# Optimization experiments

Measured on AMD Instinct MI355X. Metric: run time of the kernel, lower is better.

Reference implementation:

```python
import jax, jax.numpy as jnp
import numpy as np

GROUPS = [16, 16, 32, 64, 192]
B, H, W = 8, 64, 64


def _shift(x, dy, dx):
    # out[i, j] = x[i - dy, j - dx], zero padded (equiv. of PoolConv's depthwise shift convs)
    Hh, Ww = x.shape[-2], x.shape[-1]
    pt, pb = max(dy, 0), max(-dy, 0)
    pl, pr = max(dx, 0), max(-dx, 0)
    xp = jnp.pad(x, ((0, 0), (0, 0), (pt, pb), (pl, pr)))
    return xp[..., pb:pb + Hh, pr:pr + Ww]


def _conv5(x, w, b):
    out = jax.lax.conv_general_dilated(x, w, (1, 1), ((2, 2), (2, 2)),
                                       dimension_numbers=("NCHW", "OIHW", "NCHW"))
    return out + b[None, :, None, None]


def _fill_pool(x, m1):
    # bottom: w[0,0]=1, pad 1 -> shift down-right; top: w[2,0]=1 -> shift up-right; right: w[2,0] of 5x5, pad 2 -> shift right by 2
    xm = x * m1
    return x + _shift(xm, 1, 1) + _shift(xm, -1, 1) + _shift(xm, 0, 2)


def _forward(y, mask, sws, sbs, cws, cbs):
    m0, m1 = mask[0], mask[1]
    starts = np.cumsum([0] + GROUPS[:-1])
    outs = []
    prev = None
    for i, g in enumerate(GROUPS):
        s = y[:, int(starts[i]):int(starts[i]) + g]
        anchor = _fill_pool(s * m0, m1)
        sp = _conv5(anchor, sws[i], sbs[i]) * (1.0 - m0)
        if i == 0:
            outs.append(sp)
            prev = s
        else:
            ch = _conv5(prev, cws[i - 1], cbs[i - 1])
            outs.append(sp)
            outs.append(ch)
            prev = jnp.concatenate([prev, s], axis=1)
    return tuple(outs)


def setup_inputs() -> dict:
    key = jax.random.key(0)
    ks = jax.random.split(key, 32)
    y = jax.random.normal(ks[0], (B, sum(GROUPS), H, W), jnp.float32)
    hh, ww = jnp.meshgrid(jnp.arange(H), jnp.arange(W), indexing="ij")
    m0 = (((hh + ww) % 2) == 0).astype(jnp.float32)[None, None]  # checkerboard anchor mask
    mask = jnp.stack([m0, 1.0 - m0], axis=0)  # [2,1,1,H,W]
    starts = np.cumsum([0] + GROUPS[:-1])
    inp = {"y": y, "mask": mask, "stage": 1}
    for i, g in enumerate(GROUPS):
        inp[f"sw{i}"] = 0.02 * jax.random.normal(ks[1 + i], (2 * g, g, 5, 5), jnp.float32)
        inp[f"sb{i}"] = jnp.zeros((2 * g,), jnp.float32)
    for i in range(1, len(GROUPS)):
        inp[f"cw{i}"] = 0.02 * jax.random.normal(ks[10 + i], (2 * GROUPS[i], int(starts[i]), 5, 5), jnp.float32)
        inp[f"cb{i}"] = jnp.zeros((2 * GROUPS[i],), jnp.float32)
    return inp


def reference(y, mask, stage, sw0, sb0, sw1, sb1, sw2, sb2, sw3, sb3, sw4, sb4,
              cw1, cb1, cw2, cb2, cw3, cb3, cw4, cb4):
    # stage != TRAIN branch: AdaptiveContext returns only the conv output
    return _forward(y, mask,
                    [sw0, sw1, sw2, sw3, sw4], [sb0, sb1, sb2, sb3, sb4],
                    [cw1, cw2, cw3, cw4], [cb1, cb2, cb3, cb4])
```

## Files before the change

kernel.cpp:

```cpp
#include <hip/hip_runtime.h>

typedef __bf16 bf16_t;
typedef __bf16 bf16x8 __attribute__((ext_vector_type(8)));
typedef float f32x16 __attribute__((ext_vector_type(16)));
typedef unsigned int u32;

#define CTOT 320
#define NPIX 32768

__device__ __forceinline__ void gload16(const void* g, void* l) {
  __builtin_amdgcn_global_load_lds((const __attribute__((address_space(1))) u32*)g,
                                   (__attribute__((address_space(3))) u32*)l, 16, 0, 0);
}

__global__ __launch_bounds__(256) void k_transpose_y(const float* __restrict__ y,
                                                     bf16_t* __restrict__ yt,
                                                     bf16_t* __restrict__ ytp) {
  __shared__ bf16_t T[64][72];
  int blk = blockIdx.x;
  int c0 = (blk % 5) * 64;
  int bh = blk / 5;
  int b = bh >> 6, h = bh & 63;
  int tid = threadIdx.x;
  {
    int c = tid >> 2, w0 = (tid & 3) << 4;
    const float* src = y + (size_t)(b * CTOT + c0 + c) * 4096 + (h << 6) + w0;
#pragma unroll
    for (int j = 0; j < 16; j += 4) {
      float4 v = *(const float4*)(src + j);
      T[c][w0 + j + 0] = (bf16_t)v.x;
      T[c][w0 + j + 1] = (bf16_t)v.y;
      T[c][w0 + j + 2] = (bf16_t)v.z;
      T[c][w0 + j + 3] = (bf16_t)v.w;
    }
  }
  __syncthreads();
  {
    int w = tid >> 2, cq = (tid & 3) << 4;
    union { uint4 v; bf16_t b[8]; } u0, u1;
#pragma unroll
    for (int j = 0; j < 8; ++j) { u0.b[j] = T[cq + j][w]; u1.b[j] = T[cq + 8 + j][w]; }
    bf16_t* dst = yt + (size_t)((bh << 6) | w) * CTOT + c0 + cq;
    *(uint4*)dst = u0.v;
    *(uint4*)(dst + 8) = u1.v;
  }
  if (tid < 128) {
    int j = tid >> 2, cq = (tid & 3) << 4;
    int w = (j << 1) + (h & 1);
    union { uint4 v; bf16_t b[8]; } u0, u1;
#pragma unroll
    for (int k = 0; k < 8; ++k) { u0.b[k] = T[cq + k][w]; u1.b[k] = T[cq + 8 + k][w]; }
    bf16_t* dst = ytp + (size_t)((bh << 5) + j) * CTOT + c0 + cq;
    *(uint4*)dst = u0.v;
    *(uint4*)(dst + 8) = u1.v;
  }
}

__global__ __launch_bounds__(256) void k_transpose_w(const float* __restrict__ w,
                                                     bf16_t* __restrict__ wt,
                                                     int IC, int OC, int OCp) {
  int idx = blockIdx.x * 256 + threadIdx.x;
  if (idx >= OCp * IC) return;
  int oc = idx / IC, ic = idx - oc * IC;
  bool valid = (oc < OC);
  const float* src = w + (size_t)(oc * IC + ic) * 25;
  int icg = ic >> 3, ie = ic & 7;
#pragma unroll
  for (int t = 0; t < 25; ++t) {
    float v = valid ? src[t] : 0.0f;
    wt[(size_t)((t * (IC >> 3) + icg) * OCp + oc) * 8 + ie] = (bf16_t)v;
  }
}

__global__ void k_zero(uint4* z) { z[threadIdx.x] = uint4{0u, 0u, 0u, 0u}; }

struct ConvDesc {
  const float* bias;
  int out_off, wt_off;
  int IC, OC, OCp, chs, masked, job_start;
};
struct MainParams {
  const bf16_t* yt;
  const bf16_t* ytp;
  const bf16_t* wt;
  const bf16_t* zp;
  float* out;
  ConvDesc cv[9];
};

template <bool MASKED>
__device__ __forceinline__ void conv_run(const ConvDesc cd, const MainParams& P,
                                         int local, bf16_t* S) {
  constexpr int COLS = MASKED ? 36 : 68;
  constexpr int REAL = MASKED ? 720 : 816;
  constexpr int NSG  = MASKED ? 12 : 13;
  constexpr int SPL  = NSG * 512;
  constexpr int SINB = 2 * SPL;
  constexpr int SWO  = 2 * SINB;

  int mb = MASKED ? (local >> 5) : (local >> 6);
  int nb = local & (MASKED ? 31 : 63);
  int b  = MASKED ? (nb >> 2) : (nb >> 3);
  int hblk = MASKED ? ((nb & 3) << 4) : ((nb & 7) << 3);
  int tid = threadIdx.x, lane = tid & 63, wid = tid >> 6;
  int l31 = lane & 31, kq = lane >> 5;

  int octmax = (cd.OC - (mb << 6)) >> 5; if (octmax > 2) octmax = 2;

  f32x16 acc00 = {}, acc01 = {}, acc10 = {}, acc11 = {};

  int aofs = SWO + kq * 512 + l31 * 8;
  int bofs = kq * SPL + (MASKED ? (((wid << 1) * 36 + 1 + l31) * 8)
                                : ((wid * 68 + l31) * 8));

  const bf16_t* wtc = P.wt + cd.wt_off;
  int icgs = cd.IC >> 3;
  int nchunks = cd.IC >> 4;

  auto stage_sin = [&](int cb, int buf) {
    int ic0 = cb << 4;
    for (int g = wid; g < 2 * NSG; g += 8) {
      int p = (g >= NSG) ? 1 : 0;
      int gi = g - p * NSG;
      int s = (gi << 6) + lane;
      int rr = s / COLS, cc = s - rr * COLS;
      int h = hblk + rr - 2;
      const bf16_t* gp;
      if (!MASKED) {
        int w = cc - 2;
        bool inb = (s < REAL) && ((unsigned)h < 64u) && ((unsigned)w < 64u);
        gp = inb ? (P.yt + (size_t)((((b << 6) + (h & 63)) << 6) | (w & 63)) * CTOT
                        + cd.chs + ic0 + (p << 3))
                 : P.zp;
      } else {
        int j = cc - 1;
        bool inb = (s < REAL) && ((unsigned)h < 64u) && ((unsigned)j < 32u);
        gp = inb ? (P.ytp + (size_t)((((b << 6) + (h & 63)) << 5) + (j & 31)) * CTOT
                         + cd.chs + ic0 + (p << 3))
                 : P.zp;
      }
      gload16(gp, S + buf * SINB + p * SPL + (gi << 9));
    }
  };
  auto stage_sw = [&](int gstart, int gcnt, int swb, int cb) {
    int ic0 = cb << 4;
    for (int t = wid; t < 2 * gcnt; t += 8) {
      int slot = t >> 1, icg = t & 1;
      int ti = gstart + slot;
      int tap = MASKED ? (2 * ti + 1) : ti;
      const bf16_t* gp = wtc +
          (size_t)((tap * icgs + (ic0 >> 3) + icg) * cd.OCp + (mb << 6) + lane) * 8;
      gload16(gp, S + SWO + ((swb * 7 + slot) << 10) + (icg << 9));
    }
  };

#define TAP_ONE(TI, SL)                                                         \
    {                                                                           \
      int tap_ = MASKED ? (2 * (TI) + 1) : (TI);                                \
      int dy_ = tap_ / 5, dx_ = tap_ % 5;                                       \
      bf16x8 af0 = *(const bf16x8*)(S + aofs + (SL) * 1024);                    \
      bf16x8 bf0, bf1;                                                          \
      if (!MASKED) {                                                            \
        int toff_ = (dy_ * 68 + dx_) * 8;                                       \
        bf0 = *(const bf16x8*)(Sn + bofs + toff_);                              \
        bf1 = *(const bf16x8*)(Sn + bofs + toff_ + 256);                        \
      } else {                                                                  \
        int j0_ = (dx_ - 1 - (dy_ & 1)) / 2;                                    \
        int j1_ = (dx_ - 2 - ((dy_ + 1) & 1)) / 2;                              \
        bf0 = *(const bf16x8*)(Sn + bofs + (dy_ * 36 + j0_) * 8);               \
        bf1 = *(const bf16x8*)(Sn + bofs + ((dy_ + 1) * 36 + j1_) * 8);         \
      }                                                                         \
      acc00 = __builtin_amdgcn_mfma_f32_32x32x16_bf16(af0, bf0, acc00, 0, 0, 0);\
      acc01 = __builtin_amdgcn_mfma_f32_32x32x16_bf16(af0, bf1, acc01, 0, 0, 0);\
      if (octmax > 1) {                                                         \
        bf16x8 af1 = *(const bf16x8*)(S + aofs + (SL) * 1024 + 256);            \
        acc10 = __builtin_amdgcn_mfma_f32_32x32x16_bf16(af1, bf0, acc10, 0,0,0);\
        acc11 = __builtin_amdgcn_mfma_f32_32x32x16_bf16(af1, bf1, acc11, 0,0,0);\
      }                                                                         \
    }
#define RUNG(GS, SB, CNT)                                                       \
    _Pragma("unroll")                                                           \
    for (int s_ = 0; s_ < (CNT); ++s_) TAP_ONE((GS) + s_, (SB) + s_)

  stage_sin(0, 0);
  stage_sw(0, MASKED ? 6 : 7, 0, 0);
  for (int cb = 0; cb < nchunks; ++cb) {
    const bf16_t* Sn = S + (cb & 1) * SINB;
    __syncthreads();
    if (!MASKED) {
      stage_sw(7, 6, 1, cb);
      RUNG(0, 0, 7)
      __syncthreads();
      stage_sw(13, 6, 0, cb);
      RUNG(7, 7, 6)
      __syncthreads();
      stage_sw(19, 6, 1, cb);
      RUNG(13, 0, 6)
      __syncthreads();
      if (cb + 1 < nchunks) {
        stage_sin(cb + 1, (cb + 1) & 1);
        stage_sw(0, 7, 0, cb + 1);
      }
      RUNG(19, 7, 6)
    } else {
      stage_sw(6, 6, 1, cb);
      RUNG(0, 0, 6)
      __syncthreads();
      if (cb + 1 < nchunks) {
        stage_sin(cb + 1, (cb + 1) & 1);
        stage_sw(0, 6, 0, cb + 1);
      }
      RUNG(6, 7, 6)
    }
  }
#undef RUNG
#undef TAP_ONE

  float* outp = P.out + cd.out_off;
#define EPI_U(A, OT, PT)                                                        \
  {                                                                             \
    int h = hblk + wid;                                                         \
    _Pragma("unroll")                                                           \
    for (int r = 0; r < 16; ++r) {                                              \
      int row = (r & 3) + ((r >> 2) << 3) + (kq << 2);                          \
      int oc = (mb << 6) + ((OT) << 5) + row;                                   \
      outp[(size_t)(b * cd.OC + oc) * 4096 + (h << 6) + ((PT) << 5) + l31] =    \
          (A)[r] + cd.bias[oc];                                                 \
    }                                                                           \
  }
#define EPI_M(A, OT, PT)                                                        \
  {                                                                             \
    int h = hblk + (wid << 1) + (PT);                                           \
    _Pragma("unroll")                                                           \
    for (int r = 0; r < 16; ++r) {                                              \
      int row = (r & 3) + ((r >> 2) << 3) + (kq << 2);                          \
      int oc = (mb << 6) + ((OT) << 5) + row;                                   \
      float val = (A)[r] + cd.bias[oc];                                         \
      float2 pr;                                                                \
      if ((PT) == 0) { pr.x = 0.0f; pr.y = val; }                               \
      else           { pr.x = val;  pr.y = 0.0f; }                              \
      *(float2*)(outp + (size_t)(b * cd.OC + oc) * 4096 + (h << 6) + (l31 << 1)) = pr; \
    }                                                                           \
  }
  if (!MASKED) {
    EPI_U(acc00, 0, 0); EPI_U(acc01, 0, 1);
    if (octmax > 1) { EPI_U(acc10, 1, 0); EPI_U(acc11, 1, 1); }
  } else {
    EPI_M(acc00, 0, 0); EPI_M(acc01, 0, 1);
    if (octmax > 1) { EPI_M(acc10, 1, 0); EPI_M(acc11, 1, 1); }
  }
#undef EPI_U
#undef EPI_M
}

__global__ __launch_bounds__(512, 4) void k_conv_main(MainParams P) {
  __shared__ bf16_t S[40960];
  int bid = blockIdx.x;
  int ci = 0;
#pragma unroll
  for (int i = 1; i < 9; ++i) if (bid >= P.cv[i].job_start) ci = i;
  ConvDesc cd = P.cv[ci];
  int local = bid - cd.job_start;
  if (cd.masked) conv_run<true>(cd, P, local, S);
  else           conv_run<false>(cd, P, local, S);
}

extern "C" void kernel_launch(void* const* d_in, const int* in_sizes, int n_in,
                              void* d_out, int out_size, void* d_ws, size_t ws_size,
                              hipStream_t stream) {
  const float* y = (const float*)d_in[0];
  bf16_t* yt  = (bf16_t*)d_ws;
  bf16_t* ytp = yt + (size_t)NPIX * CTOT;
  bf16_t* wt  = ytp + (size_t)(NPIX / 2) * CTOT;
  bf16_t* zp  = wt + 3660800;

  k_transpose_y<<<2560, 256, 0, stream>>>(y, yt, ytp);
  k_zero<<<1, 64, 0, stream>>>((uint4*)zp);

  static const int ICv[9]  = {128,    192,    64,     32,     16,     64,     32,     16,    16};
  static const int OCv[9]  = {384,    384,    128,    64,     32,     128,    64,     32,    32};
  static const int OCp[9]  = {384,    384,    128,    64,     64,     128,    64,     64,    64};
  static const int WIDX[9] = {19,     11,     17,     15,     13,     9,      7,      5,     3};
  static const int BIDX[9] = {20,     12,     18,     16,     14,     10,     8,      6,     4};
  static const int CHS[9]  = {0,      128,    0,      0,      0,      64,     32,     16,    0};
  static const int MSK[9]  = {0,      1,      0,      0,      0,      1,      1,      1,     1};
  static const int WTOFF[9] = {0, 1228800, 3072000, 3276800, 3328000,
                               3353600, 3558400, 3609600, 3635200};
  static const int OUTOFF[9] = {28311552, 15728640, 11534336, 5242880, 2097152,
                                7340032,  3145728,  1048576,  0};
  static const int JOBST[9] = {0, 384, 576, 704, 768, 832, 896, 928, 960};

  for (int i = 0; i < 9; ++i) {
    int n = OCp[i] * ICv[i];
    k_transpose_w<<<(n + 255) / 256, 256, 0, stream>>>(
        (const float*)d_in[WIDX[i]], wt + WTOFF[i], ICv[i], OCv[i], OCp[i]);
  }

  MainParams P;
  P.yt = yt; P.ytp = ytp; P.wt = wt; P.zp = zp; P.out = (float*)d_out;
  for (int i = 0; i < 9; ++i) {
    P.cv[i].bias = (const float*)d_in[BIDX[i]];
    P.cv[i].out_off = OUTOFF[i];
    P.cv[i].wt_off = WTOFF[i];
    P.cv[i].IC = ICv[i]; P.cv[i].OC = OCv[i]; P.cv[i].OCp = OCp[i];
    P.cv[i].chs = CHS[i]; P.cv[i].masked = MSK[i];
    P.cv[i].job_start = JOBST[i];
  }
  k_conv_main<<<992, 512, 0, stream>>>(P);
}
```

Measured before the change: 186.8 us.

## Fuse prep kernels into one launch and split conv waves into staging roles

Merges the y transpose, the nine weight-transpose launches and the zero-fill into a single k_prep launch to cut launch overhead. In the main conv kernel, waves 0-3 now stage only input tiles and waves 4-7 stage only weights. The __syncthreads calls become raw barriers, and only the wave group that issued loads waits on vmcnt. MFMA sections are raised with s_setprio so compute waves are favoured. This relies on careful barrier correctness: each wave drains only its own loads before the barrier, which risks races if the producer/consumer ordering is wrong.

```diff
diff --git a/kernel.cpp b/kernel.cpp
--- a/kernel.cpp
+++ b/kernel.cpp
@@ -13,18 +13,51 @@
                                    (__attribute__((address_space(3))) u32*)l, 16, 0, 0);
 }
 
-__global__ __launch_bounds__(256) void k_transpose_y(const float* __restrict__ y,
-                                                     bf16_t* __restrict__ yt,
-                                                     bf16_t* __restrict__ ytp) {
+__device__ __forceinline__ void sync_drain(bool wait) {
+  if (wait) asm volatile("s_waitcnt vmcnt(0)" ::: "memory");
+  __builtin_amdgcn_sched_barrier(0);
+  __builtin_amdgcn_s_barrier();
+  __builtin_amdgcn_sched_barrier(0);
+}
+
+struct PrepParams {
+  const float* y;
+  bf16_t *yt, *ytp, *wt;
+  const float* w[9];
+  int IC[9], OC[9], OCp[9], wtoff[9], jst[9];
+  uint4* zp;
+};
+
+__global__ __launch_bounds__(256) void k_prep(PrepParams Q) {
+  int blk = blockIdx.x, tid = threadIdx.x;
+  if (blk >= 2560) {
+    int wb = blk - 2560;
+    if (wb >= 572) { if (tid < 64) Q.zp[tid] = uint4{0u, 0u, 0u, 0u}; return; }
+    int ci = 0;
+#pragma unroll
+    for (int i = 1; i < 9; ++i) if (wb >= Q.jst[i]) ci = i;
+    int IC = Q.IC[ci], OCp = Q.OCp[ci], OC = Q.OC[ci];
+    int idx = (wb - Q.jst[ci]) * 256 + tid;
+    if (idx >= OCp * IC) return;
+    int oc = idx / IC, ic = idx - oc * IC;
+    bool valid = (oc < OC);
+    const float* src = Q.w[ci] + (size_t)(oc * IC + ic) * 25;
+    bf16_t* dst = Q.wt + Q.wtoff[ci];
+    int icg = ic >> 3, ie = ic & 7;
+#pragma unroll
+    for (int t = 0; t < 25; ++t) {
+      float v = valid ? src[t] : 0.0f;
+      dst[(size_t)((t * (IC >> 3) + icg) * OCp + oc) * 8 + ie] = (bf16_t)v;
+    }
+    return;
+  }
   __shared__ bf16_t T[64][72];
-  int blk = blockIdx.x;
   int c0 = (blk % 5) * 64;
   int bh = blk / 5;
   int b = bh >> 6, h = bh & 63;
-  int tid = threadIdx.x;
   {
     int c = tid >> 2, w0 = (tid & 3) << 4;
-    const float* src = y + (size_t)(b * CTOT + c0 + c) * 4096 + (h << 6) + w0;
+    const float* src = Q.y + (size_t)(b * CTOT + c0 + c) * 4096 + (h << 6) + w0;
 #pragma unroll
     for (int j = 0; j < 16; j += 4) {
       float4 v = *(const float4*)(src + j);
@@ -40,7 +73,7 @@
     union { uint4 v; bf16_t b[8]; } u0, u1;
 #pragma unroll
     for (int j = 0; j < 8; ++j) { u0.b[j] = T[cq + j][w]; u1.b[j] = T[cq + 8 + j][w]; }
-    bf16_t* dst = yt + (size_t)((bh << 6) | w) * CTOT + c0 + cq;
+    bf16_t* dst = Q.yt + (size_t)((bh << 6) | w) * CTOT + c0 + cq;
     *(uint4*)dst = u0.v;
     *(uint4*)(dst + 8) = u1.v;
   }
@@ -50,29 +83,11 @@
     union { uint4 v; bf16_t b[8]; } u0, u1;
 #pragma unroll
     for (int k = 0; k < 8; ++k) { u0.b[k] = T[cq + k][w]; u1.b[k] = T[cq + 8 + k][w]; }
-    bf16_t* dst = ytp + (size_t)((bh << 5) + j) * CTOT + c0 + cq;
+    bf16_t* dst = Q.ytp + (size_t)((bh << 5) + j) * CTOT + c0 + cq;
     *(uint4*)dst = u0.v;
     *(uint4*)(dst + 8) = u1.v;
   }
 }
-
-__global__ __launch_bounds__(256) void k_transpose_w(const float* __restrict__ w,
-                                                     bf16_t* __restrict__ wt,
-                                                     int IC, int OC, int OCp) {
-  int idx = blockIdx.x * 256 + threadIdx.x;
-  if (idx >= OCp * IC) return;
-  int oc = idx / IC, ic = idx - oc * IC;
-  bool valid = (oc < OC);
-  const float* src = w + (size_t)(oc * IC + ic) * 25;
-  int icg = ic >> 3, ie = ic & 7;
-#pragma unroll
-  for (int t = 0; t < 25; ++t) {
-    float v = valid ? src[t] : 0.0f;
-    wt[(size_t)((t * (IC >> 3) + icg) * OCp + oc) * 8 + ie] = (bf16_t)v;
-  }
-}
-
-__global__ void k_zero(uint4* z) { z[threadIdx.x] = uint4{0u, 0u, 0u, 0u}; }
 
 struct ConvDesc {
   const float* bias;
@@ -104,6 +119,7 @@
   int hblk = MASKED ? ((nb & 3) << 4) : ((nb & 7) << 3);
   int tid = threadIdx.x, lane = tid & 63, wid = tid >> 6;
   int l31 = lane & 31, kq = lane >> 5;
+  bool sin_role = (wid < 4);
 
   int octmax = (cd.OC - (mb << 6)) >> 5; if (octmax > 2) octmax = 2;
 
@@ -119,7 +135,7 @@
 
   auto stage_sin = [&](int cb, int buf) {
     int ic0 = cb << 4;
-    for (int g = wid; g < 2 * NSG; g += 8) {
+    for (int g = wid; g < 2 * NSG; g += 4) {
       int p = (g >= NSG) ? 1 : 0;
       int gi = g - p * NSG;
       int s = (gi << 6) + lane;
@@ -144,7 +160,7 @@
   };
   auto stage_sw = [&](int gstart, int gcnt, int swb, int cb) {
     int ic0 = cb << 4;
-    for (int t = wid; t < 2 * gcnt; t += 8) {
+    for (int t = wid - 4; t < 2 * gcnt; t += 4) {
       int slot = t >> 1, icg = t & 1;
       int ti = gstart + slot;
       int tap = MASKED ? (2 * ti + 1) : ti;
@@ -179,37 +195,37 @@
       }                                                                         \
     }
 #define RUNG(GS, SB, CNT)                                                       \
+    __builtin_amdgcn_s_setprio(1);                                              \
     _Pragma("unroll")                                                           \
-    for (int s_ = 0; s_ < (CNT); ++s_) TAP_ONE((GS) + s_, (SB) + s_)
-
-  stage_sin(0, 0);
-  stage_sw(0, MASKED ? 6 : 7, 0, 0);
+    for (int s_ = 0; s_ < (CNT); ++s_) TAP_ONE((GS) + s_, (SB) + s_)            \
+    __builtin_amdgcn_s_setprio(0);
+
+  if (sin_role) stage_sin(0, 0);
+  else          stage_sw(0, MASKED ? 6 : 7, 0, 0);
+
   for (int cb = 0; cb < nchunks; ++cb) {
     const bf16_t* Sn = S + (cb & 1) * SINB;
-    __syncthreads();
+    sync_drain(true);
+    if (sin_role) {
+      if (cb + 1 < nchunks) stage_sin(cb + 1, (cb + 1) & 1);
+    }
     if (!MASKED) {
-      stage_sw(7, 6, 1, cb);
+      if (!sin_role) stage_sw(7, 6, 1, cb);
       RUNG(0, 0, 7)
-      __syncthreads();
-      stage_sw(13, 6, 0, cb);
+      sync_drain(!sin_role);
+      if (!sin_role) stage_sw(13, 6, 0, cb);
       RUNG(7, 7, 6)
-      __syncthreads();
-      stage_sw(19, 6, 1, cb);
+      sync_drain(!sin_role);
+      if (!sin_role) stage_sw(19, 6, 1, cb);
       RUNG(13, 0, 6)
-      __syncthreads();
-      if (cb + 1 < nchunks) {
-        stage_sin(cb + 1, (cb + 1) & 1);
-        stage_sw(0, 7, 0, cb + 1);
-      }
+      sync_drain(!sin_role);
+      if (!sin_role && cb + 1 < nchunks) stage_sw(0, 7, 0, cb + 1);
       RUNG(19, 7, 6)
     } else {
-      stage_sw(6, 6, 1, cb);
+      if (!sin_role) stage_sw(6, 6, 1, cb);
       RUNG(0, 0, 6)
-      __syncthreads();
-      if (cb + 1 < nchunks) {
-        stage_sin(cb + 1, (cb + 1) & 1);
-        stage_sw(0, 6, 0, cb + 1);
-      }
+      sync_drain(!sin_role);
+      if (!sin_role && cb + 1 < nchunks) stage_sw(0, 6, 0, cb + 1);
       RUNG(6, 7, 6)
     }
   }
@@ -274,9 +290,6 @@
   bf16_t* wt  = ytp + (size_t)(NPIX / 2) * CTOT;
   bf16_t* zp  = wt + 3660800;
 
-  k_transpose_y<<<2560, 256, 0, stream>>>(y, yt, ytp);
-  k_zero<<<1, 64, 0, stream>>>((uint4*)zp);
-
   static const int ICv[9]  = {128,    192,    64,     32,     16,     64,     32,     16,    16};
   static const int OCv[9]  = {384,    384,    128,    64,     32,     128,    64,     32,    32};
   static const int OCp[9]  = {384,    384,    128,    64,     64,     128,    64,     64,    64};
@@ -289,12 +302,16 @@
   static const int OUTOFF[9] = {28311552, 15728640, 11534336, 5242880, 2097152,
                                 7340032,  3145728,  1048576,  0};
   static const int JOBST[9] = {0, 384, 576, 704, 768, 832, 896, 928, 960};
-
+  static const int PJST[9] = {0, 192, 480, 512, 520, 524, 556, 564, 568};
+
+  PrepParams Q;
+  Q.y = y; Q.yt = yt; Q.ytp = ytp; Q.wt = wt; Q.zp = (uint4*)zp;
   for (int i = 0; i < 9; ++i) {
-    int n = OCp[i] * ICv[i];
-    k_transpose_w<<<(n + 255) / 256, 256, 0, stream>>>(
-        (const float*)d_in[WIDX[i]], wt + WTOFF[i], ICv[i], OCv[i], OCp[i]);
-  }
+    Q.w[i] = (const float*)d_in[WIDX[i]];
+    Q.IC[i] = ICv[i]; Q.OC[i] = OCv[i]; Q.OCp[i] = OCp[i];
+    Q.wtoff[i] = WTOFF[i]; Q.jst[i] = PJST[i];
+  }
+  k_prep<<<3133, 256, 0, stream>>>(Q);
 
   MainParams P;
   P.yt = yt; P.ytp = ytp; P.wt = wt; P.zp = zp; P.out = (float*)d_out;
```

New measurement: 157.7 us. 15.6% less time.
